# Kernel tuning notes

Measured on AMD Instinct MI355X. Metric: run time of the kernel, lower is better.

## Reference

```python
import jax, jax.numpy as jnp
import numpy as np

N_NODES = 50000
N_EDGES = 1250000
D_NODE = 64
D_EDGE = 16
D_HID = 64


def setup_inputs() -> dict:
    key = jax.random.key(0)
    ks = jax.random.split(key, 12)

    def lin(k, din, dout):
        kw, kb = jax.random.split(k)
        # lecun_normal-style init (flax Linear default kernel init)
        w = jax.random.normal(kw, (din, dout), dtype=jnp.float32) / np.sqrt(din)
        b = jnp.zeros((dout,), dtype=jnp.float32)
        return w, b

    node_features = jax.random.normal(ks[0], (N_NODES, D_NODE), dtype=jnp.float32)
    edge_features = jax.random.normal(ks[1], (N_EDGES, D_EDGE), dtype=jnp.float32)
    edge_index = jax.random.randint(ks[2], (2, N_EDGES), 0, N_NODES, dtype=jnp.int64 if jax.config.jax_enable_x64 else jnp.int32)

    w_m1, b_m1 = lin(ks[3], D_NODE + D_EDGE, D_HID)
    w_m2, b_m2 = lin(ks[4], D_HID, D_HID)
    w_u1, b_u1 = lin(ks[5], D_NODE + D_HID, D_HID)
    w_u2, b_u2 = lin(ks[6], D_HID, D_HID)

    return {
        "node_features": node_features,
        "edge_features": edge_features,
        "edge_index": edge_index,
        "w_m1": w_m1, "b_m1": b_m1,
        "w_m2": w_m2, "b_m2": b_m2,
        "w_u1": w_u1, "b_u1": b_u1,
        "w_u2": w_u2, "b_u2": b_u2,
    }


def reference(node_features, edge_features, edge_index,
              w_m1, b_m1, w_m2, b_m2, w_u1, b_u1, w_u2, b_u2):
    num_nodes = node_features.shape[0]
    src, dst = edge_index[0], edge_index[1]

    # gather source node features per edge: [E, D_NODE]
    source_features = node_features[src]
    # message MLP: [E, D_NODE+D_EDGE] -> relu -> [E, D_HID]
    msg_in = jnp.concatenate([source_features, edge_features], axis=-1)
    messages = jax.nn.relu(msg_in @ w_m1 + b_m1) @ w_m2 + b_m2

    # sum aggregation to destination nodes: [N, D_HID]
    aggregated = jax.ops.segment_sum(messages, dst, num_segments=num_nodes)

    # update MLP: [N, D_NODE+D_HID] -> relu -> [N, D_HID]
    upd_in = jnp.concatenate([node_features, aggregated], axis=-1)
    return jax.nn.relu(upd_in @ w_u1 + b_u1) @ w_u2 + b_u2
```

## Files before the change

kernel.cpp:

```cpp
#include <hip/hip_runtime.h>
#include <cstdio>


#define TPB 256

__global__ __launch_bounds__(TPB)
void GraphMessagePassing_5952824672257_kernel(
    const float* __restrict__ nodef,
    const float* __restrict__ edgef,
    const int*   __restrict__ eidx,
    const float* __restrict__ w1,
    const float* __restrict__ b1,
    const float* __restrict__ w2,
    const float* __restrict__ b2,
    float* __restrict__ agg,
    int n_edges, int n_nodes)
{
    __shared__ float HB[64][65];
    __shared__ int   SI[64];
    __shared__ int   DI[64];

    const int tid  = threadIdx.x;
    const int lane = tid & 63;
    const int wch  = __builtin_amdgcn_readfirstlane(tid >> 6) * 16;

    const long base = (long)blockIdx.x * 64;

    if (tid < 64) {
        long e  = base + tid;
        long ec = (e < n_edges) ? e : (long)n_edges - 1;
        if (ec < 0) ec = 0;
        int s  = eidx[ec];
        int dd = eidx[(size_t)n_edges + ec];
        SI[tid] = ((unsigned)s  < (unsigned)n_nodes) ? s  : 0;
        DI[tid] = ((unsigned)dd < (unsigned)n_nodes) ? dd : 0;
    }
    __syncthreads();

    const int r  = tid & 15;
    const int e0 = tid >> 4;
    int se[4];
    #pragma unroll
    for (int i = 0; i < 4; ++i) se[i] = SI[e0 + i * 16];

    float h[16];
    #pragma unroll
    for (int c = 0; c < 16; ++c) h[c] = b1[wch + c];

    #pragma unroll 1
    for (int kc = 0; kc < 5; ++kc) {
        if (kc < 4) {
            #pragma unroll
            for (int i = 0; i < 4; ++i)
                HB[r][e0 + i * 16] = nodef[(size_t)se[i] * 64 + kc * 16 + r];
        } else {
            #pragma unroll
            for (int i = 0; i < 4; ++i) {
                int flat = i * 256 + tid;
                int e  = flat >> 4, rr = flat & 15;
                long ee = base + e;
                if (ee >= n_edges) ee = n_edges - 1;
                if (ee < 0) ee = 0;
                HB[rr][e] = edgef[(size_t)ee * 16 + rr];
            }
        }
        __syncthreads();
        #pragma unroll 4
        for (int r2 = 0; r2 < 16; ++r2) {
            const float xk = HB[r2][lane];
            const float* __restrict__ wr = w1 + (kc * 16 + r2) * 64 + wch;
            #pragma unroll
            for (int c = 0; c < 16; ++c) h[c] = fmaf(xk, wr[c], h[c]);
        }
        __syncthreads();
    }

    #pragma unroll
    for (int c = 0; c < 16; ++c) HB[lane][wch + c] = fmaxf(h[c], 0.f);
    __syncthreads();

    float m[16];
    #pragma unroll
    for (int c = 0; c < 16; ++c) m[c] = b2[wch + c];
    #pragma unroll 4
    for (int t = 0; t < 64; ++t) {
        const float xt = HB[lane][t];
        const float* __restrict__ wr = w2 + t * 64 + wch;
        #pragma unroll
        for (int c = 0; c < 16; ++c) m[c] = fmaf(xt, wr[c], m[c]);
    }
    __syncthreads();

    #pragma unroll
    for (int c = 0; c < 16; ++c) HB[lane][wch + c] = m[c];
    __syncthreads();

    const int oc  = lane & 15;
    const int er4 = lane >> 4;
    #pragma unroll
    for (int g = 0; g < 16; ++g) {
        const int le = g * 4 + er4;
        const int dg = DI[le];
        const float v = HB[le][wch + oc];
        if (base + le < n_edges)
            atomicAdd(agg + (size_t)dg * 64 + wch + oc, v);
    }
}

__global__ __launch_bounds__(TPB)
void node_mlp_coop(
    const float* __restrict__ nodef,
    const float* __restrict__ agg,
    const float* __restrict__ w1,
    const float* __restrict__ b1,
    const float* __restrict__ w2,
    const float* __restrict__ b2,
    float* __restrict__ out,
    int n_nodes)
{
    __shared__ float HB[64][65];

    const int tid  = threadIdx.x;
    const int lane = tid & 63;
    const int wch  = __builtin_amdgcn_readfirstlane(tid >> 6) * 16;

    const long base = (long)blockIdx.x * 64;

    const int r  = tid & 15;
    const int e0 = tid >> 4;

    float h[16];
    #pragma unroll
    for (int c = 0; c < 16; ++c) h[c] = b1[wch + c];

    #pragma unroll 1
    for (int kc = 0; kc < 8; ++kc) {
        const float* __restrict__ src = (kc < 4) ? nodef : agg;
        const int ko = (kc & 3) * 16;
        #pragma unroll
        for (int i = 0; i < 4; ++i) {
            long row = base + e0 + i * 16;
            if (row >= n_nodes) row = n_nodes - 1;
            if (row < 0) row = 0;
            HB[r][e0 + i * 16] = src[(size_t)row * 64 + ko + r];
        }
        __syncthreads();
        #pragma unroll 4
        for (int r2 = 0; r2 < 16; ++r2) {
            const float xk = HB[r2][lane];
            const float* __restrict__ wr = w1 + (kc * 16 + r2) * 64 + wch;
            #pragma unroll
            for (int c = 0; c < 16; ++c) h[c] = fmaf(xk, wr[c], h[c]);
        }
        __syncthreads();
    }

    #pragma unroll
    for (int c = 0; c < 16; ++c) HB[lane][wch + c] = fmaxf(h[c], 0.f);
    __syncthreads();

    float m[16];
    #pragma unroll
    for (int c = 0; c < 16; ++c) m[c] = b2[wch + c];
    #pragma unroll 4
    for (int t = 0; t < 64; ++t) {
        const float xt = HB[lane][t];
        const float* __restrict__ wr = w2 + t * 64 + wch;
        #pragma unroll
        for (int c = 0; c < 16; ++c) m[c] = fmaf(xt, wr[c], m[c]);
    }
    __syncthreads();

    #pragma unroll
    for (int c = 0; c < 16; ++c) HB[lane][wch + c] = m[c];
    __syncthreads();

    const int oc  = lane & 15;
    const int er4 = lane >> 4;
    #pragma unroll
    for (int g = 0; g < 16; ++g) {
        const int le = g * 4 + er4;
        const float v = HB[le][wch + oc];
        if (base + le < n_nodes)
            out[(size_t)(base + le) * 64 + wch + oc] = v;
    }
}

extern "C" void kernel_launch(void* const* d_in, const int* in_sizes, int n_in,
                              void* d_out, int out_size, void* d_ws, size_t ws_size,
                              hipStream_t stream) {
    const float* nodef = (const float*)d_in[0];
    const float* edgef = (const float*)d_in[1];
    const int*   eidx  = (const int*)d_in[2];
    const float* w_m1  = (const float*)d_in[3];
    const float* b_m1  = (const float*)d_in[4];
    const float* w_m2  = (const float*)d_in[5];
    const float* b_m2  = (const float*)d_in[6];
    const float* w_u1  = (const float*)d_in[7];
    const float* b_u1  = (const float*)d_in[8];
    const float* w_u2  = (const float*)d_in[9];
    const float* b_u2  = (const float*)d_in[10];
    float* out = (float*)d_out;

    const int n_nodes = out_size / 64;
    const int n_edges = in_sizes[2] / 2;
    if (n_edges <= 0 || n_nodes <= 0) return;

    fprintf(stderr, "[KL] f32 4-wave-coop E=%d N=%d ws=%zu\n",
            n_edges, n_nodes, ws_size);
    fflush(stderr);

    float* agg = (float*)d_ws;
    hipMemsetAsync(agg, 0, (size_t)n_nodes * 64 * sizeof(float), stream);

    const int blocks_e = (n_edges + 63) / 64;
    GraphMessagePassing_5952824672257_kernel<<<blocks_e, TPB, 0, stream>>>(
        nodef, edgef, eidx, w_m1, b_m1, w_m2, b_m2, agg, n_edges, n_nodes);

    const int blocks_n = (n_nodes + 63) / 64;
    node_mlp_coop<<<blocks_n, TPB, 0, stream>>>(
        nodef, agg, w_u1, b_u1, w_u2, b_u2, out, n_nodes);

    hipError_t le = hipGetLastError();
    fprintf(stderr, "[KL] last=%d(%s)\n", (int)le, hipGetErrorName(le));
    fflush(stderr);
}
```

Baseline: 481.6 us.

## Double-buffer gathered input chunks in LDS with register prefetch

Both the edge-message kernel and the node-update kernel now use two LDS buffers for the 16-wide input chunks. The next chunk is loaded into registers while the current chunk's FMAs run, and it is written to the other buffer afterwards. This cuts one barrier per iteration and hides global gather latency behind compute. The cost is extra registers for the prefetch values and offsets, and fully unrolled loops that may increase register pressure.

```diff
diff --git a/kernel.cpp b/kernel.cpp
--- a/kernel.cpp
+++ b/kernel.cpp
@@ -19,6 +19,7 @@
     __shared__ float HB[64][65];
     __shared__ int   SI[64];
     __shared__ int   DI[64];
+    float* __restrict__ Xf = &HB[0][0];
 
     const int tid  = threadIdx.x;
     const int lane = tid & 63;
@@ -43,37 +44,64 @@
     #pragma unroll
     for (int i = 0; i < 4; ++i) se[i] = SI[e0 + i * 16];
 
+    int    xoff4[4];
+    size_t goff4[4];
+    #pragma unroll
+    for (int i = 0; i < 4; ++i) {
+        int flat = i * 256 + tid;
+        int e = flat >> 4, rr = flat & 15;
+        long ee = base + e;
+        if (ee >= n_edges) ee = n_edges - 1;
+        if (ee < 0) ee = 0;
+        xoff4[i] = rr * 66 + e;
+        goff4[i] = (size_t)ee * 16 + rr;
+    }
+
     float h[16];
     #pragma unroll
     for (int c = 0; c < 16; ++c) h[c] = b1[wch + c];
 
-    #pragma unroll 1
+    float pf[4];
+    #pragma unroll
+    for (int i = 0; i < 4; ++i) pf[i] = nodef[(size_t)se[i] * 64 + r];
+    #pragma unroll
+    for (int i = 0; i < 4; ++i) Xf[r * 66 + e0 + i * 16] = pf[i];
+    #pragma unroll
+    for (int i = 0; i < 4; ++i) pf[i] = nodef[(size_t)se[i] * 64 + 16 + r];
+    __syncthreads();
+
+    #pragma unroll
     for (int kc = 0; kc < 5; ++kc) {
-        if (kc < 4) {
-            #pragma unroll
-            for (int i = 0; i < 4; ++i)
-                HB[r][e0 + i * 16] = nodef[(size_t)se[i] * 64 + kc * 16 + r];
-        } else {
-            #pragma unroll
-            for (int i = 0; i < 4; ++i) {
-                int flat = i * 256 + tid;
-                int e  = flat >> 4, rr = flat & 15;
-                long ee = base + e;
-                if (ee >= n_edges) ee = n_edges - 1;
-                if (ee < 0) ee = 0;
-                HB[rr][e] = edgef[(size_t)ee * 16 + rr];
-            }
-        }
-        __syncthreads();
+        const int cur = kc & 1;
         #pragma unroll 4
         for (int r2 = 0; r2 < 16; ++r2) {
-            const float xk = HB[r2][lane];
+            const float xk = Xf[cur * 1056 + r2 * 66 + lane];
             const float* __restrict__ wr = w1 + (kc * 16 + r2) * 64 + wch;
             #pragma unroll
             for (int c = 0; c < 16; ++c) h[c] = fmaf(xk, wr[c], h[c]);
         }
-        __syncthreads();
-    }
+        if (kc < 4) {
+            if (kc == 3) {
+                #pragma unroll
+                for (int i = 0; i < 4; ++i)
+                    Xf[(cur ^ 1) * 1056 + xoff4[i]] = pf[i];
+            } else {
+                #pragma unroll
+                for (int i = 0; i < 4; ++i)
+                    Xf[(cur ^ 1) * 1056 + r * 66 + e0 + i * 16] = pf[i];
+            }
+            if (kc == 2) {
+                #pragma unroll
+                for (int i = 0; i < 4; ++i) pf[i] = edgef[goff4[i]];
+            } else if (kc < 2) {
+                #pragma unroll
+                for (int i = 0; i < 4; ++i)
+                    pf[i] = nodef[(size_t)se[i] * 64 + (kc + 2) * 16 + r];
+            }
+            __syncthreads();
+        }
+    }
+    __syncthreads();
 
     #pragma unroll
     for (int c = 0; c < 16; ++c) HB[lane][wch + c] = fmaxf(h[c], 0.f);
@@ -119,6 +147,7 @@
     int n_nodes)
 {
     __shared__ float HB[64][65];
+    float* __restrict__ Xf = &HB[0][0];
 
     const int tid  = threadIdx.x;
     const int lane = tid & 63;
@@ -128,32 +157,52 @@
 
     const int r  = tid & 15;
     const int e0 = tid >> 4;
+    size_t rows[4];
+    #pragma unroll
+    for (int i = 0; i < 4; ++i) {
+        long row = base + e0 + i * 16;
+        if (row >= n_nodes) row = n_nodes - 1;
+        if (row < 0) row = 0;
+        rows[i] = (size_t)row * 64;
+    }
 
     float h[16];
     #pragma unroll
     for (int c = 0; c < 16; ++c) h[c] = b1[wch + c];
 
-    #pragma unroll 1
+    float pf[4];
+    #pragma unroll
+    for (int i = 0; i < 4; ++i) pf[i] = nodef[rows[i] + r];
+    #pragma unroll
+    for (int i = 0; i < 4; ++i) Xf[r * 66 + e0 + i * 16] = pf[i];
+    #pragma unroll
+    for (int i = 0; i < 4; ++i) pf[i] = nodef[rows[i] + 16 + r];
+    __syncthreads();
+
+    #pragma unroll
     for (int kc = 0; kc < 8; ++kc) {
-        const float* __restrict__ src = (kc < 4) ? nodef : agg;
-        const int ko = (kc & 3) * 16;
-        #pragma unroll
-        for (int i = 0; i < 4; ++i) {
-            long row = base + e0 + i * 16;
-            if (row >= n_nodes) row = n_nodes - 1;
-            if (row < 0) row = 0;
-            HB[r][e0 + i * 16] = src[(size_t)row * 64 + ko + r];
-        }
-        __syncthreads();
+        const int cur = kc & 1;
         #pragma unroll 4
         for (int r2 = 0; r2 < 16; ++r2) {
-            const float xk = HB[r2][lane];
+            const float xk = Xf[cur * 1056 + r2 * 66 + lane];
             const float* __restrict__ wr = w1 + (kc * 16 + r2) * 64 + wch;
             #pragma unroll
             for (int c = 0; c < 16; ++c) h[c] = fmaf(xk, wr[c], h[c]);
         }
-        __syncthreads();
-    }
+        if (kc < 7) {
+            #pragma unroll
+            for (int i = 0; i < 4; ++i)
+                Xf[(cur ^ 1) * 1056 + r * 66 + e0 + i * 16] = pf[i];
+            if (kc < 6) {
+                const float* __restrict__ src = (kc + 2 < 4) ? nodef : agg;
+                const int ko = ((kc + 2) & 3) * 16;
+                #pragma unroll
+                for (int i = 0; i < 4; ++i) pf[i] = src[rows[i] + ko + r];
+            }
+            __syncthreads();
+        }
+    }
+    __syncthreads();
 
     #pragma unroll
     for (int c = 0; c < 16; ++c) HB[lane][wch + c] = fmaxf(h[c], 0.f);
@@ -206,7 +255,7 @@
     const int n_edges = in_sizes[2] / 2;
     if (n_edges <= 0 || n_nodes <= 0) return;
 
-    fprintf(stderr, "[KL] f32 4-wave-coop E=%d N=%d ws=%zu\n",
+    fprintf(stderr, "[KL] f32 4-wave-coop dbuf E=%d N=%d ws=%zu\n",
             n_edges, n_nodes, ws_size);
     fflush(stderr);
 
```

After: 465.0 us. -3.4%, faster.
